# Optimization experiments

Measured on AMD Instinct MI355X. Metric: run time of the kernel, lower is better.

Reference implementation:

```python
import jax, jax.numpy as jnp
import numpy as np

EPS = 1e-8
LAMBDA_SOFTMAX = 9.0   # opt.lambda_softmax (SCAN t2i default)
ITERATION_STEP = 2     # opt.iteration_step
LEAKY_SLOPE = 0.1      # clipped_l2norm leaky relu slope


def l2norm(x, axis):
    norm = jnp.sqrt(jnp.sum(x * x, axis=axis, keepdims=True)) + EPS
    return x / norm


def cosine_sim(a, b, axis):
    w12 = jnp.sum(a * b, axis=axis)
    w1 = jnp.linalg.norm(a, axis=axis)
    w2 = jnp.linalg.norm(b, axis=axis)
    return w12 / jnp.clip(w1 * w2, EPS)


def func_attention_t2i(query, context):
    """query: [C, I, T, D] caption words per (caption, image) pair;
    context: [I, R, D] image regions. Returns weightedContext [C, I, T, D]."""
    # attn = bmm(context, query^T) -> [C, I, R, T]
    attn = jnp.einsum('ird,citd->cirt', context, query)
    # raw_feature_norm == 'clipped_l2norm': LeakyReLU(0.1) then l2norm over queryL
    attn = jax.nn.leaky_relu(attn, LEAKY_SLOPE)
    attn = l2norm(attn, axis=-1)
    # transpose -> [C, I, T, R]; temperature softmax over sourceL (regions)
    attn = jnp.swapaxes(attn, -1, -2)
    attn = jax.nn.softmax(attn * LAMBDA_SOFTMAX, axis=-1)
    # weightedContext = bmm(context^T, attn^T)^T -> [C, I, T, D]
    return jnp.einsum('citr,ird->citd', attn, context)


def setup_inputs() -> dict:
    key = jax.random.key(0)
    ks = jax.random.split(key, 4)
    B, R, T, D = 32, 36, 40, 1024
    # encoder outputs are l2-normalized along the feature dim
    img_emb = l2norm(jax.random.normal(ks[0], (B, R, D), jnp.float32), axis=-1)
    cap_emb = l2norm(jax.random.normal(ks[1], (B, T, D), jnp.float32), axis=-1)
    W_lin = jax.random.normal(ks[2], (2 * D, D), jnp.float32) * 0.02
    b_lin = jnp.zeros((D,), jnp.float32)
    W_gate = jax.random.normal(ks[3], (2 * D, D), jnp.float32) * 0.02
    b_gate = jnp.zeros((D,), jnp.float32)
    return dict(img_emb=img_emb, cap_emb=cap_emb,
                W_lin=W_lin, b_lin=b_lin, W_gate=W_gate, b_gate=b_gate)


def reference(img_emb, cap_emb, W_lin, b_lin, W_gate, b_gate):
    """xattn_score_Text_IMRAM (t2i) with gated memory, summed over iterations.
    Returns similarity score matrix [n_image, n_caption]."""
    C, T, D = cap_emb.shape
    I = img_emb.shape[0]
    # cap_i_expand: each caption repeated across all images
    cap_exp = jnp.broadcast_to(cap_emb[:, None], (C, I, T, D))
    query = cap_exp
    score = jnp.zeros((I, C), cap_emb.dtype)
    for _ in range(ITERATION_STEP):
        wc = func_attention_t2i(query, img_emb)            # [C, I, T, D]
        # cosine similarity per word vs original caption words, mean over words
        row_sim = cosine_sim(cap_exp, wc, axis=-1).mean(-1)  # [C, I]
        score = score + row_sim.T                           # [I, C]
        # gated_memory_t2i
        cat = jnp.concatenate([query, wc], axis=-1)         # [C, I, T, 2D]
        upd = jnp.tanh(cat @ W_lin + b_lin)
        gate = jax.nn.sigmoid(cat @ W_gate + b_gate)
        query = query * gate + upd * (1.0 - gate)
    return score
```

## Files before the change

### kernel.cpp

```cpp
#include <hip/hip_runtime.h>
#include <stdint.h>


typedef unsigned short u16;
typedef __attribute__((ext_vector_type(8))) short bf16x8;
typedef __attribute__((ext_vector_type(4))) float f32x4;

#define MFMA_BF16(a, b, c) __builtin_amdgcn_mfma_f32_16x16x32_bf16((a), (b), (c), 0, 0, 0)

__device__ __forceinline__ float bf2f(u16 u) {
  union { unsigned v; float f; } x; x.v = ((unsigned)u) << 16; return x.f;
}
__device__ __forceinline__ u16 f2bf(float f) {
  union { float f; unsigned v; } x; x.f = f;
  return (u16)((x.v + 0x7fffu + ((x.v >> 16) & 1u)) >> 16);
}
__device__ __forceinline__ float frcp(float x) { return __builtin_amdgcn_rcpf(x); }
__device__ __forceinline__ void gl2lds16(const u16* g, u16* l) {
  __builtin_amdgcn_global_load_lds((const __attribute__((address_space(1))) void*)g,
                                   (__attribute__((address_space(3))) void*)l, 16, 0, 0);
}

__device__ __forceinline__ size_t fragIdx(int ct, int d) {
  const int tile = ct >> 5, nt = (ct >> 4) & 1, l15 = ct & 15;
  const int dc = d >> 7, wvd = (d >> 5) & 3, mt = (d >> 4) & 1;
  const int quad = (d >> 2) & 3, rg = d & 3;
  const int lane = quad * 16 + l15;
  return ((((((size_t)tile * 8 + dc) * 4 + wvd) * 2 + mt) * 2 + nt) * 64 + lane) * 4 + rg;
}

__global__ void prep_k(const float* __restrict__ img, const float* __restrict__ cap,
                       const float* __restrict__ Wl, const float* __restrict__ Wg,
                       u16* __restrict__ imgb, u16* __restrict__ capb,
                       u16* __restrict__ capP,
                       u16* __restrict__ WTl, u16* __restrict__ WTg,
                       float* __restrict__ cnorm, u16* __restrict__ cwF0) {
  __shared__ u16 tile[32][33];
  const int b = blockIdx.x, tid = threadIdx.x;
  if (b < 1152) {
    const int idx = (b * 256 + tid) * 4;
    const float4 v = *(const float4*)(img + idx);
    u16 o[4] = {f2bf(v.x), f2bf(v.y), f2bf(v.z), f2bf(v.w)};
    *(uint2*)(imgb + idx) = *(const uint2*)o;
  } else if (b < 2432) {
    const int idx = ((b - 1152) * 256 + tid) * 4;
    const float4 v = *(const float4*)(cap + idx);
    u16 o[4] = {f2bf(v.x), f2bf(v.y), f2bf(v.z), f2bf(v.w)};
    *(uint2*)(capb + idx) = *(const uint2*)o;
    const int ct = idx >> 10, d0 = idx & 1023;
    *(uint2*)(capP + fragIdx(ct, d0)) = *(const uint2*)o;
  } else if (b < 6528) {
    const int b2 = b - 2432;
    const int bx = b2 & 63, by = (b2 >> 6) & 31, bz = b2 >> 11;
    const float* src = bz ? Wg : Wl;
    u16* dst = bz ? WTg : WTl;
    const int k0 = bx * 32, n0 = by * 32;
    const int tx = tid & 31, ty = tid >> 5;
#pragma unroll
    for (int j = 0; j < 4; ++j)
      tile[ty + 8 * j][tx] = f2bf(src[(size_t)(k0 + ty + 8 * j) * 1024 + n0 + tx]);
    __syncthreads();
#pragma unroll
    for (int j = 0; j < 4; ++j)
      dst[(size_t)(n0 + ty + 8 * j) * 2048 + k0 + tx] = tile[tx][ty + 8 * j];
  } else if (b < 6848) {
    const int wv = tid >> 6, lane = tid & 63;
    const int row = (b - 6528) * 4 + wv;
    const float* p = cap + ((size_t)row << 10) + lane * 16;
    float s = 0.f;
#pragma unroll
    for (int e = 0; e < 16; ++e) { float v = p[e]; s += v * v; }
#pragma unroll
    for (int off = 32; off > 0; off >>= 1) s += __shfl_down(s, off, 64);
    if (lane == 0) cnorm[row] = sqrtf(s);
  } else {
    const int idx = ((b - 6848) * 256 + tid) * 8;
    uint4 z; z.x = z.y = z.z = z.w = 0u;
    *(uint4*)(cwF0 + idx) = z;
  }
}

__global__ __launch_bounds__(256, 2) void gemms_k(
    const u16* __restrict__ capb, const u16* __restrict__ imgb,
    const u16* __restrict__ WTl, const u16* __restrict__ WTg,
    u16* __restrict__ prePL, u16* __restrict__ prePG,
    u16* __restrict__ cwFL, u16* __restrict__ cwFG,
    const float* __restrict__ bL, const float* __restrict__ bG,
    float* __restrict__ S1, u16* __restrict__ Ghi, u16* __restrict__ Glo) {
  __shared__ __align__(16) char lsU[20480];
  const int bid = blockIdx.x;
  const int tid = threadIdx.x;
  const int wv = tid >> 6, lane = tid & 63;
  const int quad = lane >> 4, l15 = lane & 15;
  const bf16x8 zero8 = {0, 0, 0, 0, 0, 0, 0, 0};

  if (bid < 640) {
    u16* lsA = (u16*)lsU;
    u16* lsB = (u16*)(lsU + 4096);
    const int i = bid & 31, m0 = (bid >> 5) * 64;
    const u16* B = imgb + (size_t)i * 36 * 1024;
    f32x4 acc[3];
#pragma unroll
    for (int b = 0; b < 3; ++b) acc[b] = (f32x4){0.f, 0.f, 0.f, 0.f};
    for (int kt = 0; kt < 32; ++kt) {
      if (kt) __syncthreads();
      const int rr = tid >> 2, j = tid & 3;
      const int js = j ^ ((rr >> 2) & 3);
      gl2lds16(capb + (size_t)(m0 + rr) * 1024 + kt * 32 + js * 8,
               lsA + (size_t)(wv * 64) * 8);
      const int rc = rr < 36 ? rr : 35;
      gl2lds16(B + (size_t)rc * 1024 + kt * 32 + js * 8,
               lsB + (size_t)(wv * 64) * 8);
      __syncthreads();
      const int ra = wv * 16 + l15;
      const bf16x8 a2 = *(const bf16x8*)(lsA + ra * 32 + (quad ^ ((ra >> 2) & 3)) * 8);
      bf16x8 b3[3];
#pragma unroll
      for (int nf = 0; nf < 3; ++nf) {
        const int rb = nf * 16 + l15;
        const bf16x8 bv = *(const bf16x8*)(lsB + rb * 32 + (quad ^ ((rb >> 2) & 3)) * 8);
        b3[nf] = (rb < 36) ? bv : zero8;
      }
#pragma unroll
      for (int nf = 0; nf < 3; ++nf) acc[nf] = MFMA_BF16(a2, b3[nf], acc[nf]);
    }
#pragma unroll
    for (int nf = 0; nf < 3; ++nf)
#pragma unroll
      for (int rg = 0; rg < 4; ++rg) {
        const int m = m0 + wv * 16 + quad * 4 + rg;
        S1[((size_t)i * 1280 + m) * 48 + nf * 16 + l15] = acc[nf][rg];
      }
  } else if (bid < 944) {
    u16* lsA = (u16*)lsU;
    u16* lsBl = (u16*)(lsU + 4096);
    u16* lsBg = (u16*)(lsU + 12288);
    const int b2 = bid - 640;
    const int bm = b2 >> 3, bn = b2 & 7;
    const bool iscap = bm < 20;
    const u16* A = iscap ? capb + (size_t)bm * 64 * 1024
                         : imgb + (size_t)(bm - 20) * 64 * 1024;
    const int kofs = iscap ? 0 : 1024;
    const int wm = (wv & 1) * 32, wn = (wv >> 1) * 64;
    f32x4 accL[2][4], accG[2][4];
#pragma unroll
    for (int a = 0; a < 2; ++a)
#pragma unroll
      for (int b = 0; b < 4; ++b) {
        accL[a][b] = (f32x4){0.f, 0.f, 0.f, 0.f};
        accG[a][b] = (f32x4){0.f, 0.f, 0.f, 0.f};
      }
    for (int kt = 0; kt < 32; ++kt) {
      if (kt) __syncthreads();
      {
        const int row = tid >> 2, c8 = tid & 3;
        const int js = c8 ^ (row & 3);
        gl2lds16(A + (size_t)row * 1024 + kt * 32 + js * 8,
                 lsA + (size_t)(wv * 64) * 8);
      }
#pragma unroll
      for (int s = 0; s < 2; ++s) {
        const int idx = s * 256 + tid;
        const int row = idx >> 2, c8 = idx & 3;
        const int js = c8 ^ (row & 3);
        const size_t bro = (size_t)(bn * 128 + row) * 2048 + kofs + kt * 32 + js * 8;
        gl2lds16(WTl + bro, lsBl + (size_t)(s * 256 + wv * 64) * 8);
        gl2lds16(WTg + bro, lsBg + (size_t)(s * 256 + wv * 64) * 8);
      }
      __syncthreads();
      bf16x8 af[2], bl8[4], bg8[4];
#pragma unroll
      for (int mt = 0; mt < 2; ++mt) {
        const int ra = wm + mt * 16 + l15;
        af[mt] = *(const bf16x8*)(lsA + ra * 32 + (quad ^ (ra & 3)) * 8);
      }
#pragma unroll
      for (int nt = 0; nt < 4; ++nt) {
        const int rb = wn + nt * 16 + l15;
        const int off = rb * 32 + (quad ^ (rb & 3)) * 8;
        bl8[nt] = *(const bf16x8*)(lsBl + off);
        bg8[nt] = *(const bf16x8*)(lsBg + off);
      }
#pragma unroll
      for (int mt = 0; mt < 2; ++mt)
#pragma unroll
        for (int nt = 0; nt < 4; ++nt) {
          accL[mt][nt] = MFMA_BF16(af[mt], bl8[nt], accL[mt][nt]);
          accG[mt][nt] = MFMA_BF16(af[mt], bg8[nt], accG[mt][nt]);
        }
    }
#pragma unroll
    for (int mt = 0; mt < 2; ++mt)
#pragma unroll
      for (int nt = 0; nt < 4; ++nt) {
        const int n = bn * 128 + wn + nt * 16 + l15;
        if (iscap) {
          const float blv = bL[n], bgv = bG[n];
#pragma unroll
          for (int r = 0; r < 4; ++r) {
            const int m = bm * 64 + wm + mt * 16 + quad * 4 + r;
            const size_t fi = fragIdx(m, n);
            prePL[fi] = f2bf(accL[mt][nt][r] + blv);
            prePG[fi] = f2bf(accG[mt][nt][r] + bgv);
          }
        } else {
          const int db = n >> 4, l15d = n & 15;
#pragma unroll
          for (int r = 0; r < 4; ++r) {
            const int mi = (bm - 20) * 64 + wm + mt * 16 + quad * 4 + r;
            const int i = (mi * 3641) >> 17;
            const int r36 = mi - i * 36;
            const int ksr = r36 >> 5, qd = (r36 & 31) >> 3, e = r36 & 7;
            const size_t gb =
                ((((size_t)i * 64 + db) * 2 + ksr) * 64 + qd * 16 + l15d) * 8 + e;
            cwFL[gb] = f2bf(accL[mt][nt][r]);
            cwFG[gb] = f2bf(accG[mt][nt][r]);
          }
        }
      }
  } else {
    float* lsS = (float*)lsU;
    const int i = bid - 944;
    for (int k = tid; k < 48 * 52; k += 256) lsS[k] = 0.f;
    const u16* arow[3]; bool avalid[3];
#pragma unroll
    for (int mt = 0; mt < 3; ++mt) {
      const int r = mt * 16 + l15;
      avalid[mt] = r < 36;
      arow[mt] = imgb + ((size_t)(i * 36 + (r < 36 ? r : 35)) << 10);
    }
    f32x4 acc[3][3];
#pragma unroll
    for (int a = 0; a < 3; ++a)
#pragma unroll
      for (int b = 0; b < 3; ++b) acc[a][b] = (f32x4){0.f, 0.f, 0.f, 0.f};
    for (int kk = wv * 8; kk < wv * 8 + 8; ++kk) {
      const int ko = kk * 32 + quad * 8;
      bf16x8 af[3];
#pragma unroll
      for (int mt = 0; mt < 3; ++mt)
        af[mt] = avalid[mt] ? *(const bf16x8*)(arow[mt] + ko) : zero8;
#pragma unroll
      for (int mt = 0; mt < 3; ++mt)
#pragma unroll
        for (int nt = 0; nt < 3; ++nt)
          acc[mt][nt] = MFMA_BF16(af[mt], af[nt], acc[mt][nt]);
    }
    __syncthreads();
#pragma unroll
    for (int mt = 0; mt < 3; ++mt)
#pragma unroll
      for (int nt = 0; nt < 3; ++nt)
#pragma unroll
        for (int rg = 0; rg < 4; ++rg)
          atomicAdd(&lsS[(nt * 16 + l15) * 52 + mt * 16 + quad * 4 + rg],
                    acc[mt][nt][rg]);
    __syncthreads();
    if (wv == 0) {
#pragma unroll
      for (int nt = 0; nt < 3; ++nt) {
        const int rp = nt * 16 + l15;
#pragma unroll
        for (int mt = 0; mt < 3; ++mt) {
          const f32x4 g = *(const f32x4*)&lsS[rp * 52 + mt * 16 + quad * 4];
          u16 hv[4], lv[4];
#pragma unroll
          for (int rg = 0; rg < 4; ++rg) {
            hv[rg] = f2bf(g[rg]);
            lv[rg] = f2bf(g[rg] - bf2f(hv[rg]));
          }
          const size_t gb = ((size_t)i * 48 + rp) * 64 + mt * 16 + quad * 4;
          *(uint2*)(Ghi + gb) = *(const uint2*)hv;
          *(uint2*)(Glo + gb) = *(const uint2*)lv;
        }
      }
    }
    for (int k = tid; k < 48 * 16; k += 256) {
      const size_t gb = ((size_t)i * 48 + (k >> 4)) * 64 + 48 + (k & 15);
      Ghi[gb] = 0; Glo[gb] = 0;
    }
  }
}

__global__ __launch_bounds__(256, 4) void gates2_k(
    const u16* __restrict__ cwFL, const u16* __restrict__ cwFG,
    const u16* __restrict__ P1, const u16* __restrict__ prePL,
    const u16* __restrict__ prePG, const u16* __restrict__ capP,
    const u16* __restrict__ imgb, float* __restrict__ S2) {
  __shared__ __align__(16) float lsS2f[32 * 52];
  const int tid = threadIdx.x;
  const int bid = blockIdx.x;
  const int i = bid & 31, ctt = bid >> 5;
  const int ct0 = ctt * 32;
  const int wv = tid >> 6, lane = tid & 63;
  const int quad = lane >> 4, l15 = lane & 15;

  for (int k = tid; k < 32 * 52; k += 256) lsS2f[k] = 0.f;
  __syncthreads();

  bf16x8 bp[2][2];
#pragma unroll
  for (int nt = 0; nt < 2; ++nt)
#pragma unroll
    for (int ks = 0; ks < 2; ++ks)
      bp[nt][ks] = *(const bf16x8*)(
          P1 + ((size_t)i * 1280 + ct0 + nt * 16 + l15) * 64 + ks * 32 + quad * 8);

  const u16* arow[3]; bool avalid[3];
#pragma unroll
  for (int mt = 0; mt < 3; ++mt) {
    const int r = mt * 16 + l15;
    avalid[mt] = r < 36;
    arow[mt] = imgb + ((size_t)(i * 36 + (r < 36 ? r : 35)) << 10);
  }
  const bf16x8 zero8 = {0, 0, 0, 0, 0, 0, 0, 0};

  f32x4 acc2[3][2];
#pragma unroll
  for (int a = 0; a < 3; ++a)
#pragma unroll
    for (int b = 0; b < 2; ++b) acc2[a][b] = (f32x4){0.f, 0.f, 0.f, 0.f};

  for (int dc = 0; dc < 8; ++dc) {
    f32x4 accL[2][2], accG[2][2];
#pragma unroll
    for (int a = 0; a < 2; ++a)
#pragma unroll
      for (int b = 0; b < 2; ++b) {
        accL[a][b] = (f32x4){0.f, 0.f, 0.f, 0.f};
        accG[a][b] = (f32x4){0.f, 0.f, 0.f, 0.f};
      }
#pragma unroll
    for (int mt = 0; mt < 2; ++mt)
#pragma unroll
      for (int ks = 0; ks < 2; ++ks) {
        const int db = dc * 8 + wv * 2 + mt;
        const size_t co = ((((size_t)i * 64 + db) * 2 + ks) * 64 + lane) * 8;
        const bf16x8 al = *(const bf16x8*)(cwFL + co);
        const bf16x8 ag = *(const bf16x8*)(cwFG + co);
#pragma unroll
        for (int nt = 0; nt < 2; ++nt) {
          accL[mt][nt] = MFMA_BF16(al, bp[nt][ks], accL[mt][nt]);
          accG[mt][nt] = MFMA_BF16(ag, bp[nt][ks], accG[mt][nt]);
        }
      }

    const size_t fb = (((size_t)ctt * 8 + dc) * 4 + wv) * 2;
    uint2 ovv[2][2];
#pragma unroll
    for (int mt = 0; mt < 2; ++mt) {
#pragma unroll
      for (int nt = 0; nt < 2; ++nt) {
        const size_t fo = (((fb + mt) * 2 + nt) * 64 + lane) * 4;
        const uint2 plv = *(const uint2*)(prePL + fo);
        const uint2 pgv = *(const uint2*)(prePG + fo);
        const uint2 cfv = *(const uint2*)(capP + fo);
        const float pl4[4] = {bf2f((u16)(plv.x & 0xffffu)), bf2f((u16)(plv.x >> 16)),
                              bf2f((u16)(plv.y & 0xffffu)), bf2f((u16)(plv.y >> 16))};
        const float pg4[4] = {bf2f((u16)(pgv.x & 0xffffu)), bf2f((u16)(pgv.x >> 16)),
                              bf2f((u16)(pgv.y & 0xffffu)), bf2f((u16)(pgv.y >> 16))};
        const float cf4[4] = {bf2f((u16)(cfv.x & 0xffffu)), bf2f((u16)(cfv.x >> 16)),
                              bf2f((u16)(cfv.y & 0xffffu)), bf2f((u16)(cfv.y >> 16))};
        u16 ov[4];
#pragma unroll
        for (int rg = 0; rg < 4; ++rg) {
          const float aL = accL[mt][nt][rg] + pl4[rg];
          const float aG = accG[mt][nt][rg] + pg4[rg];
          const float g = frcp(1.f + __expf(-aG));
          const float u = 2.f * frcp(1.f + __expf(-2.f * aL)) - 1.f;
          ov[rg] = f2bf(cf4[rg] * g + u * (1.f - g));
        }
        ovv[mt][nt] = *(const uint2*)ov;
      }
    }

#pragma unroll
    for (int nt = 0; nt < 2; ++nt) {
      unsigned w[4];
#pragma unroll
      for (int j2 = 0; j2 < 4; ++j2) {
        const int srcl = ((quad & 1) * 2 + (j2 >> 1)) * 16 + l15;
        const unsigned a0 =
            __shfl((j2 & 1) ? ovv[0][nt].y : ovv[0][nt].x, srcl, 64);
        const unsigned a1 =
            __shfl((j2 & 1) ? ovv[1][nt].y : ovv[1][nt].x, srcl, 64);
        w[j2] = (quad >= 2) ? a1 : a0;
      }
      union { unsigned u[4]; bf16x8 v; } bq;
      bq.u[0] = w[0]; bq.u[1] = w[1]; bq.u[2] = w[2]; bq.u[3] = w[3];
      const int dg = dc * 128 + wv * 32 + quad * 8;
#pragma unroll
      for (int mt = 0; mt < 3; ++mt) {
        const bf16x8 af = avalid[mt] ? *(const bf16x8*)(arow[mt] + dg) : zero8;
        acc2[mt][nt] = MFMA_BF16(af, bq.v, acc2[mt][nt]);
      }
    }
  }
#pragma unroll
  for (int mt = 0; mt < 3; ++mt)
#pragma unroll
    for (int nt = 0; nt < 2; ++nt)
#pragma unroll
      for (int rg = 0; rg < 4; ++rg)
        atomicAdd(&lsS2f[(nt * 16 + l15) * 52 + mt * 16 + quad * 4 + rg],
                  acc2[mt][nt][rg]);
  __syncthreads();
  for (int idx = tid; idx < 384; idx += 256) {
    const int ct = idx / 12, rq = idx % 12;
    *(f32x4*)(S2 + ((size_t)i * 1280 + ct0 + ct) * 48 + rq * 4) =
        *(const f32x4*)&lsS2f[ct * 52 + rq * 4];
  }
}

template <int PASS2>
__global__ __launch_bounds__(256, 2) void score_k(
    const float* __restrict__ Ssm, const float* __restrict__ S1,
    const u16* __restrict__ Ghi, const u16* __restrict__ Glo,
    const float* __restrict__ cnorm, u16* __restrict__ P1,
    float* __restrict__ sim1, float* __restrict__ score) {
  __shared__ __align__(16) u16 lsP[4][48 * 72];
  const int tid = threadIdx.x;
  const int wv = tid >> 6, lane = tid & 63;
  const int quad = lane >> 4, l15 = lane & 15;
  const int pair = blockIdx.x * 4 + wv;
  const int c = pair >> 5, i = pair & 31;
  u16* lsPw = lsP[wv];
  for (int k = lane; k < 1728; k += 64) ((unsigned*)lsPw)[k] = 0u;

  float sS[3][3][4], s1f[3][3][4];
  const float* Sb = Ssm + ((size_t)i * 1280 + c * 40) * 48;
  const float* S1b = S1 + ((size_t)i * 1280 + c * 40) * 48;
#pragma unroll
  for (int nt = 0; nt < 3; ++nt) {
    const int t = nt * 16 + l15;
    const int tr = t < 40 ? t : 39;
#pragma unroll
    for (int mt = 0; mt < 3; ++mt) {
      f32x4 v = *(const f32x4*)(Sb + (size_t)tr * 48 + mt * 16 + quad * 4);
      if (t >= 40) v = (f32x4){0.f, 0.f, 0.f, 0.f};
#pragma unroll
      for (int rg = 0; rg < 4; ++rg) sS[mt][nt][rg] = v[rg];
      if (PASS2) {
        const f32x4 w = *(const f32x4*)(S1b + (size_t)tr * 48 + mt * 16 + quad * 4);
#pragma unroll
        for (int rg = 0; rg < 4; ++rg) s1f[mt][nt][rg] = w[rg];
      } else {
#pragma unroll
        for (int rg = 0; rg < 4; ++rg) s1f[mt][nt][rg] = v[rg];
      }
    }
  }

  float rn[3][4];
#pragma unroll
  for (int mt = 0; mt < 3; ++mt)
#pragma unroll
    for (int rg = 0; rg < 4; ++rg) {
      float s2 = 0.f;
#pragma unroll
      for (int nt = 0; nt < 3; ++nt) {
        float v = sS[mt][nt][rg]; v = v > 0.f ? v : 0.1f * v; s2 += v * v;
      }
      s2 += __shfl_xor(s2, 1, 64); s2 += __shfl_xor(s2, 2, 64);
      s2 += __shfl_xor(s2, 4, 64); s2 += __shfl_xor(s2, 8, 64);
      rn[mt][rg] = sqrtf(s2) + 1e-8f;
    }
  float mx[3] = {-3.0e38f, -3.0e38f, -3.0e38f};
#pragma unroll
  for (int mt = 0; mt < 3; ++mt)
#pragma unroll
    for (int nt = 0; nt < 3; ++nt)
#pragma unroll
      for (int rg = 0; rg < 4; ++rg) {
        const int r = mt * 16 + quad * 4 + rg;
        float v = sS[mt][nt][rg]; v = v > 0.f ? v : 0.1f * v;
        float zz = 9.f * v / rn[mt][rg];
        zz = (r < 36) ? zz : -3.0e38f;
        sS[mt][nt][rg] = zz;
        mx[nt] = fmaxf(mx[nt], zz);
      }
#pragma unroll
  for (int nt = 0; nt < 3; ++nt) {
    mx[nt] = fmaxf(mx[nt], __shfl_xor(mx[nt], 16, 64));
    mx[nt] = fmaxf(mx[nt], __shfl_xor(mx[nt], 32, 64));
  }
  float ss[3] = {0.f, 0.f, 0.f};
#pragma unroll
  for (int mt = 0; mt < 3; ++mt)
#pragma unroll
    for (int nt = 0; nt < 3; ++nt)
#pragma unroll
      for (int rg = 0; rg < 4; ++rg) {
        const float e = __expf(sS[mt][nt][rg] - mx[nt]);
        sS[mt][nt][rg] = e; ss[nt] += e;
      }
#pragma unroll
  for (int nt = 0; nt < 3; ++nt) {
    ss[nt] += __shfl_xor(ss[nt], 16, 64);
    ss[nt] += __shfl_xor(ss[nt], 32, 64);
    ss[nt] = 1.f / ss[nt];
  }
#pragma unroll
  for (int nt = 0; nt < 3; ++nt) {
    const int t = nt * 16 + l15;
#pragma unroll
    for (int mt = 0; mt < 3; ++mt) {
#pragma unroll
      for (int rg = 0; rg < 4; ++rg) sS[mt][nt][rg] *= ss[nt];
      if (t < 40) {
        u16 pv[4];
#pragma unroll
        for (int rg = 0; rg < 4; ++rg) pv[rg] = f2bf(sS[mt][nt][rg]);
        *(uint2*)(lsPw + t * 72 + mt * 16 + quad * 4) = *(const uint2*)pv;
      }
    }
  }

  float pnv[3] = {0.f, 0.f, 0.f};
#pragma unroll
  for (int nt = 0; nt < 3; ++nt)
#pragma unroll
    for (int mt = 0; mt < 3; ++mt)
#pragma unroll
      for (int rg = 0; rg < 4; ++rg) pnv[nt] += sS[mt][nt][rg] * s1f[mt][nt][rg];

  if (!PASS2) {
    for (int idx = lane; idx < 320; idx += 64) {
      const int t = idx >> 3, j = idx & 7;
      *(uint4*)(P1 + ((size_t)i * 1280 + c * 40 + t) * 64 + j * 8) =
          *(const uint4*)(lsPw + t * 72 + j * 8);
    }
  }

  bf16x8 afA[3][2];
#pragma unroll
  for (int mtT = 0; mtT < 3; ++mtT)
#pragma unroll
    for (int ks = 0; ks < 2; ++ks)
      afA[mtT][ks] =
          *(const bf16x8*)(lsPw + (mtT * 16 + l15) * 72 + ks * 32 + quad * 8);
  f32x4 gp[3][3];
#pragma unroll
  for (int a = 0; a < 3; ++a)
#pragma unroll
    for (int b = 0; b < 3; ++b) gp[a][b] = (f32x4){0.f, 0.f, 0.f, 0.f};
#pragma unroll
  for (int ks = 0; ks < 2; ++ks)
#pragma unroll
    for (int mtG = 0; mtG < 3; ++mtG) {
      const size_t gb = ((size_t)i * 48 + mtG * 16 + l15) * 64 + ks * 32 + quad * 8;
      const bf16x8 gh = *(const bf16x8*)(Ghi + gb);
      const bf16x8 gl = *(const bf16x8*)(Glo + gb);
#pragma unroll
      for (int mtT = 0; mtT < 3; ++mtT) {
        gp[mtG][mtT] = MFMA_BF16(gh, afA[mtT][ks], gp[mtG][mtT]);
        gp[mtG][mtT] = MFMA_BF16(gl, afA[mtT][ks], gp[mtG][mtT]);
      }
    }
  float pwv[3] = {0.f, 0.f, 0.f};
#pragma unroll
  for (int nt = 0; nt < 3; ++nt)
#pragma unroll
    for (int mt = 0; mt < 3; ++mt)
#pragma unroll
      for (int rg = 0; rg < 4; ++rg)
        pwv[nt] += sS[mt][nt][rg] * gp[mt][nt][rg];
#pragma unroll
  for (int nt = 0; nt < 3; ++nt) {
    pnv[nt] += __shfl_xor(pnv[nt], 16, 64); pnv[nt] += __shfl_xor(pnv[nt], 32, 64);
    pwv[nt] += __shfl_xor(pwv[nt], 16, 64); pwv[nt] += __shfl_xor(pwv[nt], 32, 64);
  }
  float tot = 0.f;
#pragma unroll
  for (int nt = 0; nt < 3; ++nt) {
    const int t = nt * 16 + l15;
    if (t < 40) {
      const float w2 = sqrtf(fmaxf(pwv[nt], 0.f));
      tot += pnv[nt] / fmaxf(cnorm[c * 40 + t] * w2, 1e-8f);
    }
  }
  tot += __shfl_xor(tot, 1, 64); tot += __shfl_xor(tot, 2, 64);
  tot += __shfl_xor(tot, 4, 64); tot += __shfl_xor(tot, 8, 64);
  if (lane == 0) {
    const float s = tot * (1.f / 40.f);
    if (PASS2) score[i * 32 + c] = sim1[pair] + s;
    else sim1[pair] = s;
  }
}

extern "C" void kernel_launch(void* const* d_in, const int* in_sizes, int n_in,
                              void* d_out, int out_size, void* d_ws, size_t ws_size,
                              hipStream_t stream) {
  const float* img = (const float*)d_in[0];
  const float* cap = (const float*)d_in[1];
  const float* Wl  = (const float*)d_in[2];
  const float* bl  = (const float*)d_in[3];
  const float* Wg  = (const float*)d_in[4];
  const float* bg  = (const float*)d_in[5];
  float* out = (float*)d_out;

  char* ws = (char*)d_ws;
  float* cnrm = (float*)ws;               ws += 5120;
  float* sim1 = (float*)ws;               ws += 4096;
  u16*   WTl  = (u16*)ws;                 ws += (size_t)1024 * 2048 * 2;
  u16*   WTg  = (u16*)ws;                 ws += (size_t)1024 * 2048 * 2;
  u16*   prePL= (u16*)ws;                 ws += (size_t)1280 * 1024 * 2;
  u16*   prePG= (u16*)ws;                 ws += (size_t)1280 * 1024 * 2;
  u16*   capb = (u16*)ws;                 ws += (size_t)1280 * 1024 * 2;
  u16*   capP = (u16*)ws;                 ws += (size_t)1280 * 1024 * 2;
  u16*   imgb = (u16*)ws;                 ws += (size_t)1152 * 1024 * 2;
  u16*   Ghi  = (u16*)ws;                 ws += (size_t)32 * 48 * 64 * 2;
  u16*   Glo  = (u16*)ws;                 ws += (size_t)32 * 48 * 64 * 2;
  u16*   cwFL = (u16*)ws;                 ws += (size_t)32 * 64 * 2 * 64 * 8 * 2;
  u16*   cwFG = (u16*)ws;                 ws += (size_t)32 * 64 * 2 * 64 * 8 * 2;
  float* S1   = (float*)ws;               ws += (size_t)32 * 1280 * 48 * 4;
  float* S2   = (float*)ws;               ws += (size_t)32 * 1280 * 48 * 4;
  u16*   P1   = (u16*)ws;                 ws += (size_t)32 * 1280 * 64 * 2;

  prep_k<<<8896, 256, 0, stream>>>(img, cap, Wl, Wg, imgb, capb, capP,
                                   WTl, WTg, cnrm, cwFL);
  gemms_k<<<976, 256, 0, stream>>>(capb, imgb, WTl, WTg, prePL, prePG,
                                   cwFL, cwFG, bl, bg, S1, Ghi, Glo);
  score_k<0><<<256, 256, 0, stream>>>(S1, S1, Ghi, Glo, cnrm, P1, sim1, out);
  gates2_k<<<1280, 256, 0, stream>>>(cwFL, cwFG, P1, prePL, prePG, capP,
                                     imgb, S2);
  score_k<1><<<256, 256, 0, stream>>>(S2, S1, Ghi, Glo, cnrm, P1, sim1, out);
}
```

Before: 236.7 us.

## Split gates2 over feature-dim halves and pre-swizzle image into MFMA fragments

```diff
diff --git a/kernel.cpp b/kernel.cpp
--- a/kernel.cpp
+++ b/kernel.cpp
@@ -32,7 +32,7 @@
 __global__ void prep_k(const float* __restrict__ img, const float* __restrict__ cap,
                        const float* __restrict__ Wl, const float* __restrict__ Wg,
                        u16* __restrict__ imgb, u16* __restrict__ capb,
-                       u16* __restrict__ capP,
+                       u16* __restrict__ capP, u16* __restrict__ imgF,
                        u16* __restrict__ WTl, u16* __restrict__ WTg,
                        float* __restrict__ cnorm, u16* __restrict__ cwF0) {
   __shared__ u16 tile[32][33];
@@ -73,10 +73,29 @@
 #pragma unroll
     for (int off = 32; off > 0; off >>= 1) s += __shfl_down(s, off, 64);
     if (lane == 0) cnorm[row] = sqrtf(s);
-  } else {
+  } else if (b < 8896) {
     const int idx = ((b - 6848) * 256 + tid) * 8;
     uint4 z; z.x = z.y = z.z = z.w = 0u;
     *(uint4*)(cwF0 + idx) = z;
+  } else {
+    const int g = (b - 8896) * 256 + tid;
+    const int i = g / 6144, rem = g - i * 6144;
+    const int mt = rem >> 11, rem2 = rem & 2047;
+    const int w = rem2 >> 6, lane = rem2 & 63;
+    const int r = mt * 16 + (lane & 15);
+    const int d = w * 32 + (lane >> 4) * 8;
+    u16 o[8];
+    if (r < 36) {
+      const float* p = img + (((size_t)(i * 36 + r)) << 10) + d;
+      const float4 v0 = *(const float4*)p;
+      const float4 v1 = *(const float4*)(p + 4);
+      o[0] = f2bf(v0.x); o[1] = f2bf(v0.y); o[2] = f2bf(v0.z); o[3] = f2bf(v0.w);
+      o[4] = f2bf(v1.x); o[5] = f2bf(v1.y); o[6] = f2bf(v1.z); o[7] = f2bf(v1.w);
+    } else {
+#pragma unroll
+      for (int e = 0; e < 8; ++e) o[e] = 0;
+    }
+    *(uint4*)(imgF + (size_t)g * 8) = *(const uint4*)o;
   }
 }
 
@@ -286,11 +305,12 @@
     const u16* __restrict__ cwFL, const u16* __restrict__ cwFG,
     const u16* __restrict__ P1, const u16* __restrict__ prePL,
     const u16* __restrict__ prePG, const u16* __restrict__ capP,
-    const u16* __restrict__ imgb, float* __restrict__ S2) {
+    const u16* __restrict__ imgF, float* __restrict__ S2a,
+    float* __restrict__ S2b) {
   __shared__ __align__(16) float lsS2f[32 * 52];
   const int tid = threadIdx.x;
   const int bid = blockIdx.x;
-  const int i = bid & 31, ctt = bid >> 5;
+  const int dh = bid & 1, i = (bid >> 1) & 31, ctt = bid >> 6;
   const int ct0 = ctt * 32;
   const int wv = tid >> 6, lane = tid & 63;
   const int quad = lane >> 4, l15 = lane & 15;
@@ -306,22 +326,13 @@
       bp[nt][ks] = *(const bf16x8*)(
           P1 + ((size_t)i * 1280 + ct0 + nt * 16 + l15) * 64 + ks * 32 + quad * 8);
 
-  const u16* arow[3]; bool avalid[3];
-#pragma unroll
-  for (int mt = 0; mt < 3; ++mt) {
-    const int r = mt * 16 + l15;
-    avalid[mt] = r < 36;
-    arow[mt] = imgb + ((size_t)(i * 36 + (r < 36 ? r : 35)) << 10);
-  }
-  const bf16x8 zero8 = {0, 0, 0, 0, 0, 0, 0, 0};
-
   f32x4 acc2[3][2];
 #pragma unroll
   for (int a = 0; a < 3; ++a)
 #pragma unroll
     for (int b = 0; b < 2; ++b) acc2[a][b] = (f32x4){0.f, 0.f, 0.f, 0.f};
 
-  for (int dc = 0; dc < 8; ++dc) {
+  for (int dc = dh * 4; dc < dh * 4 + 4; ++dc) {
     f32x4 accL[2][2], accG[2][2];
 #pragma unroll
     for (int a = 0; a < 2; ++a)
@@ -388,10 +399,11 @@
       }
       union { unsigned u[4]; bf16x8 v; } bq;
       bq.u[0] = w[0]; bq.u[1] = w[1]; bq.u[2] = w[2]; bq.u[3] = w[3];
-      const int dg = dc * 128 + wv * 32 + quad * 8;
+      const int wn = dc * 4 + wv;
 #pragma unroll
       for (int mt = 0; mt < 3; ++mt) {
-        const bf16x8 af = avalid[mt] ? *(const bf16x8*)(arow[mt] + dg) : zero8;
+        const bf16x8 af = *(const bf16x8*)(
+            imgF + ((((size_t)i * 3 + mt) * 32 + wn) * 64 + lane) * 8);
         acc2[mt][nt] = MFMA_BF16(af, bq.v, acc2[mt][nt]);
       }
     }
@@ -405,16 +417,18 @@
         atomicAdd(&lsS2f[(nt * 16 + l15) * 52 + mt * 16 + quad * 4 + rg],
                   acc2[mt][nt][rg]);
   __syncthreads();
+  float* S2h = dh ? S2b : S2a;
   for (int idx = tid; idx < 384; idx += 256) {
     const int ct = idx / 12, rq = idx % 12;
-    *(f32x4*)(S2 + ((size_t)i * 1280 + ct0 + ct) * 48 + rq * 4) =
+    *(f32x4*)(S2h + ((size_t)i * 1280 + ct0 + ct) * 48 + rq * 4) =
         *(const f32x4*)&lsS2f[ct * 52 + rq * 4];
   }
 }
 
 template <int PASS2>
 __global__ __launch_bounds__(256, 2) void score_k(
-    const float* __restrict__ Ssm, const float* __restrict__ S1,
+    const float* __restrict__ Ssm, const float* __restrict__ SsmB,
+    const float* __restrict__ S1,
     const u16* __restrict__ Ghi, const u16* __restrict__ Glo,
     const float* __restrict__ cnorm, u16* __restrict__ P1,
     float* __restrict__ sim1, float* __restrict__ score) {
@@ -429,6 +443,7 @@
 
   float sS[3][3][4], s1f[3][3][4];
   const float* Sb = Ssm + ((size_t)i * 1280 + c * 40) * 48;
+  const float* Sb2 = SsmB + ((size_t)i * 1280 + c * 40) * 48;
   const float* S1b = S1 + ((size_t)i * 1280 + c * 40) * 48;
 #pragma unroll
   for (int nt = 0; nt < 3; ++nt) {
@@ -437,6 +452,10 @@
 #pragma unroll
     for (int mt = 0; mt < 3; ++mt) {
       f32x4 v = *(const f32x4*)(Sb + (size_t)tr * 48 + mt * 16 + quad * 4);
+      if (PASS2) {
+        const f32x4 vb = *(const f32x4*)(Sb2 + (size_t)tr * 48 + mt * 16 + quad * 4);
+        v += vb;
+      }
       if (t >= 40) v = (f32x4){0.f, 0.f, 0.f, 0.f};
 #pragma unroll
       for (int rg = 0; rg < 4; ++rg) sS[mt][nt][rg] = v[rg];
@@ -609,20 +628,22 @@
   u16*   capb = (u16*)ws;                 ws += (size_t)1280 * 1024 * 2;
   u16*   capP = (u16*)ws;                 ws += (size_t)1280 * 1024 * 2;
   u16*   imgb = (u16*)ws;                 ws += (size_t)1152 * 1024 * 2;
+  u16*   imgF = (u16*)ws;                 ws += (size_t)32 * 3 * 32 * 64 * 8 * 2;
   u16*   Ghi  = (u16*)ws;                 ws += (size_t)32 * 48 * 64 * 2;
   u16*   Glo  = (u16*)ws;                 ws += (size_t)32 * 48 * 64 * 2;
   u16*   cwFL = (u16*)ws;                 ws += (size_t)32 * 64 * 2 * 64 * 8 * 2;
   u16*   cwFG = (u16*)ws;                 ws += (size_t)32 * 64 * 2 * 64 * 8 * 2;
   float* S1   = (float*)ws;               ws += (size_t)32 * 1280 * 48 * 4;
-  float* S2   = (float*)ws;               ws += (size_t)32 * 1280 * 48 * 4;
+  float* S2a  = (float*)ws;               ws += (size_t)32 * 1280 * 48 * 4;
+  float* S2b  = (float*)ws;               ws += (size_t)32 * 1280 * 48 * 4;
   u16*   P1   = (u16*)ws;                 ws += (size_t)32 * 1280 * 64 * 2;
 
-  prep_k<<<8896, 256, 0, stream>>>(img, cap, Wl, Wg, imgb, capb, capP,
+  prep_k<<<9664, 256, 0, stream>>>(img, cap, Wl, Wg, imgb, capb, capP, imgF,
                                    WTl, WTg, cnrm, cwFL);
   gemms_k<<<976, 256, 0, stream>>>(capb, imgb, WTl, WTg, prePL, prePG,
                                    cwFL, cwFG, bl, bg, S1, Ghi, Glo);
-  score_k<0><<<256, 256, 0, stream>>>(S1, S1, Ghi, Glo, cnrm, P1, sim1, out);
-  gates2_k<<<1280, 256, 0, stream>>>(cwFL, cwFG, P1, prePL, prePG, capP,
-                                     imgb, S2);
-  score_k<1><<<256, 256, 0, stream>>>(S2, S1, Ghi, Glo, cnrm, P1, sim1, out);
-}
+  score_k<0><<<256, 256, 0, stream>>>(S1, S1, S1, Ghi, Glo, cnrm, P1, sim1, out);
+  gates2_k<<<2560, 256, 0, stream>>>(cwFL, cwFG, P1, prePL, prePG, capP,
+                                     imgF, S2a, S2b);
+  score_k<1><<<256, 256, 0, stream>>>(S2a, S2b, S1, Ghi, Glo, cnrm, P1, sim1, out);
+}
```

New measurement: 258.9 us. 9.3% more time.
